# Optimization experiments

Hardware: AMD Instinct MI355X
Metric: run time of the kernel (lower is better)

The kernel has to match this reference:

```python
import jax, jax.numpy as jnp
import numpy as np

HEADS = 16
DIM_HEAD = 64
WINDOW = 128
LOOK_BACKWARD = 1
LOOK_FORWARD = 0
THETA = 10000.0
PAD_VALUE = -1


def look_around(x, backward, forward, pad_value, axis):
    """Gather overlapping windows: concat shifted copies along the intra-window axis."""
    w = x.shape[axis]
    size = backward + forward + 1
    pads = [(0, 0)] * x.ndim
    pads[axis] = (backward, forward)
    p = jnp.pad(x, pads, constant_values=pad_value)
    segs = [jax.lax.slice_in_dim(p, s, s + w, axis=axis) for s in range(size)]
    return jnp.concatenate(segs, axis=axis + 1)


def rotate_half(t):
    t1, t2 = jnp.split(t, 2, axis=-1)
    return jnp.concatenate([-t2, t1], axis=-1)


def setup_inputs() -> dict:
    key = jax.random.key(0)
    k1, k2, k3 = jax.random.split(key, 3)
    dim = 1024
    x = jax.random.normal(k1, (4, 4096, dim), dtype=jnp.float32)
    W_qkv = jax.random.normal(k2, (dim, 3 * HEADS * DIM_HEAD), dtype=jnp.float32) * (dim ** -0.5)
    W_out = jax.random.normal(k3, (HEADS * DIM_HEAD, dim), dtype=jnp.float32) * ((HEADS * DIM_HEAD) ** -0.5)
    return {"x": x, "W_qkv": W_qkv, "W_out": W_out}


def reference(x, W_qkv, W_out):
    b, n, dim = x.shape
    h, dh, ws = HEADS, DIM_HEAD, WINDOW
    w = n // ws
    j = ws * (LOOK_BACKWARD + LOOK_FORWARD + 1)  # 256 keys per query window

    qkv = x @ W_qkv  # (b, n, 3*h*dh)
    q, k, v = jnp.split(qkv, 3, axis=-1)

    def to_bhwnd(t):
        return t.reshape(b, n, h, dh).transpose(0, 2, 1, 3).reshape(b, h, w, ws, dh)

    bq = to_bhwnd(q) * (dh ** -0.5)
    bk = look_around(to_bhwnd(k), LOOK_BACKWARD, LOOK_FORWARD, float(PAD_VALUE), axis=2)
    bv = look_around(to_bhwnd(v), LOOK_BACKWARD, LOOK_FORWARD, float(PAD_VALUE), axis=2)

    # rotary embeddings over the look-around key length; queries use last ws positions
    inv_freq = 1.0 / (THETA ** (jnp.arange(0, dh, 2, dtype=jnp.float32) / dh))
    t_pos = jnp.arange(j, dtype=jnp.float32)
    freqs = t_pos[:, None] * inv_freq[None, :]
    freqs = jnp.concatenate([freqs, freqs], axis=-1)  # (j, dh)
    q_freqs = freqs[-ws:]
    bq = bq * jnp.cos(q_freqs) + rotate_half(bq) * jnp.sin(q_freqs)
    bk = bk * jnp.cos(freqs) + rotate_half(bk) * jnp.sin(freqs)

    sim = jnp.einsum('bhwid,bhwjd->bhwij', bq, bk)  # (b,h,w,ws,j)

    seq = jnp.arange(n).reshape(w, ws)
    bq_t = seq[:, :, None]  # (w, ws, 1)
    bq_k = look_around(seq[None], LOOK_BACKWARD, LOOK_FORWARD, PAD_VALUE, axis=1)[0]  # (w, j)
    bq_k = bq_k[:, None, :]  # (w, 1, j)
    pad_mask = bq_k == PAD_VALUE
    # causal + exact window (look_backward * window_size)
    causal_mask = (bq_t < bq_k) | (bq_t > bq_k + ws * LOOK_BACKWARD)
    mask = causal_mask | pad_mask

    mask_value = -jnp.finfo(sim.dtype).max
    sim = jnp.where(mask, mask_value, sim)
    attn = jax.nn.softmax(sim, axis=-1)

    out = jnp.einsum('bhwij,bhwjd->bhwid', attn, bv)
    out = out.reshape(b, h, n, dh).transpose(0, 2, 1, 3).reshape(b, n, h * dh)
    return out @ W_out
```

## Files before the change

### kernel.cpp

```cpp
#include <hip/hip_runtime.h>
#include <stdint.h>


typedef __attribute__((ext_vector_type(8))) short bfrag;
typedef __attribute__((ext_vector_type(4))) float f4;

#define MFMA_BF16(a, b, c) __builtin_amdgcn_mfma_f32_16x16x32_bf16((a), (b), (c), 0, 0, 0)

static __device__ __forceinline__ short f2bf(float f) {
  unsigned u = __builtin_bit_cast(unsigned, f);
  u = (u + 0x7fffu + ((u >> 16) & 1u)) >> 16;
  return (short)u;
}
static __device__ __forceinline__ float bf2f(short s) {
  unsigned u = ((unsigned)(unsigned short)s) << 16;
  return __builtin_bit_cast(float, u);
}

typedef __attribute__((address_space(3))) unsigned lds_u;
typedef __attribute__((address_space(1))) unsigned gbl_u;

static __device__ __forceinline__ void gl_lds16(const void* g, const void* lds) {
  unsigned loff = (unsigned)__builtin_amdgcn_readfirstlane((int)(uintptr_t)lds);
  __builtin_amdgcn_global_load_lds((gbl_u*)(uintptr_t)g, (lds_u*)(uintptr_t)loff, 16, 0, 0);
}

__global__ __launch_bounds__(256) void convert_x(const float* __restrict__ x,
                                                 short* __restrict__ xb) {
  int idx = blockIdx.x * 256 + threadIdx.x;
  size_t base = (size_t)idx * 8;
  float4 a = *(const float4*)(x + base);
  float4 b = *(const float4*)(x + base + 4);
  bfrag o;
  o[0] = f2bf(a.x); o[1] = f2bf(a.y); o[2] = f2bf(a.z); o[3] = f2bf(a.w);
  o[4] = f2bf(b.x); o[5] = f2bf(b.y); o[6] = f2bf(b.z); o[7] = f2bf(b.w);
  *(bfrag*)(xb + base) = o;
}

__global__ __launch_bounds__(256) void transpose_w(
    const float* __restrict__ wqkv, const float* __restrict__ wout,
    short* __restrict__ wqkvT, short* __restrict__ woutT) {
  __shared__ short t[64][72];
  const int tid = threadIdx.x;
  const int kt = blockIdx.x, yt = blockIdx.y;
  const float* src; short* dst; int N, nt;
  if (yt < 48) { src = wqkv; dst = wqkvT; N = 3072; nt = yt; }
  else         { src = wout; dst = woutT; N = 1024; nt = yt - 48; }
  const int k0 = kt * 64, n0 = nt * 64;
#pragma unroll
  for (int i = 0; i < 4; ++i) {
    int r = i * 16 + (tid >> 4);
    int c = (tid & 15) * 4;
    float4 v = *(const float4*)(src + (size_t)(k0 + r) * N + n0 + c);
    t[c + 0][r] = f2bf(v.x);
    t[c + 1][r] = f2bf(v.y);
    t[c + 2][r] = f2bf(v.z);
    t[c + 3][r] = f2bf(v.w);
  }
  __syncthreads();
#pragma unroll
  for (int i = 0; i < 2; ++i) {
    int c = tid + i * 256;
    int n = c >> 3, k8 = (c & 7) * 8;
    *(bfrag*)(dst + (size_t)(n0 + n) * 1024 + k0 + k8) = *(const bfrag*)&t[n][k8];
  }
}

#define VM4 asm volatile("s_waitcnt vmcnt(4)" ::: "memory")
#define VM0 asm volatile("s_waitcnt vmcnt(0)" ::: "memory")
#define VNOP ((void)0)

#define ST_A(buf, ks, kk)                                                          \
  do {                                                                             \
    gl_lds16(aS0 + (ks) * 32 + (kk), ldsA + (buf) * 32768 + (ks) * 16384 + stA);   \
    gl_lds16(aS1 + (ks) * 32 + (kk),                                               \
             ldsA + (buf) * 32768 + (ks) * 16384 + 8192 + stA);                    \
  } while (0)
#define ST_B(buf, ks, kk)                                                          \
  do {                                                                             \
    gl_lds16(bS0 + (ks) * 32 + (kk), ldsB + (buf) * 32768 + (ks) * 16384 + stA);   \
    gl_lds16(bS1 + (ks) * 32 + (kk),                                               \
             ldsB + (buf) * 32768 + (ks) * 16384 + 8192 + stA);                    \
  } while (0)
#define ST2(buf, ks, kk) do { ST_A(buf, ks, kk); ST_B(buf, ks, kk); } while (0)

#define MM4(mi, a)                                 \
  acc[mi][0] = MFMA_BF16(a, b0, acc[mi][0]);       \
  acc[mi][1] = MFMA_BF16(a, b1, acc[mi][1]);       \
  acc[mi][2] = MFMA_BF16(a, b2, acc[mi][2]);       \
  acc[mi][3] = MFMA_BF16(a, b3, acc[mi][3])

#define PHASE2(buf, ks, STAGE, WAIT)                                               \
  {                                                                                \
    const char* pA_ = ldsA + (buf) * 32768 + (ks) * 16384 + aRd;                   \
    const char* pB_ = ldsB + (buf) * 32768 + (ks) * 16384 + bRd;                   \
    bfrag a0 = *(const bfrag*)(pA_);                                               \
    bfrag a1 = *(const bfrag*)(pA_ + 1024);                                        \
    bfrag a2 = *(const bfrag*)(pA_ + 2048);                                        \
    bfrag a3 = *(const bfrag*)(pA_ + 3072);                                        \
    bfrag a4 = *(const bfrag*)(pA_ + 4096);                                        \
    bfrag a5 = *(const bfrag*)(pA_ + 5120);                                        \
    bfrag a6 = *(const bfrag*)(pA_ + 6144);                                        \
    bfrag a7 = *(const bfrag*)(pA_ + 7168);                                        \
    bfrag b0 = *(const bfrag*)(pB_);                                               \
    bfrag b1 = *(const bfrag*)(pB_ + 1024);                                        \
    bfrag b2 = *(const bfrag*)(pB_ + 2048);                                        \
    bfrag b3 = *(const bfrag*)(pB_ + 3072);                                        \
    STAGE;                                                                         \
    WAIT;                                                                          \
    __builtin_amdgcn_s_barrier();                                                  \
    asm volatile("s_waitcnt lgkmcnt(0)" ::: "memory");                             \
    __builtin_amdgcn_sched_barrier(0);                                             \
    __builtin_amdgcn_s_setprio(1);                                                 \
    MM4(0, a0);                                                                    \
    MM4(1, a1);                                                                    \
    MM4(2, a2);                                                                    \
    MM4(3, a3);                                                                    \
    MM4(4, a4);                                                                    \
    MM4(5, a5);                                                                    \
    MM4(6, a6);                                                                    \
    MM4(7, a7);                                                                    \
    __builtin_amdgcn_s_setprio(0);                                                 \
  }

template <int MODE, int NBX>
__global__ __launch_bounds__(512, 2) void gemm256(
    const short* __restrict__ A, const short* __restrict__ Bt, float* __restrict__ C,
    short* __restrict__ oq, short* __restrict__ ok, short* __restrict__ ov) {
  __shared__ __align__(1024) char lds[131072];
  char* const ldsA = lds;
  char* const ldsB = lds + 65536;

  const int tid = threadIdx.x, lane = tid & 63, wv = tid >> 6;
  const int wr = wv >> 2, wc = wv & 3;
  const int l15 = lane & 15, quad = lane >> 4;

  const int nwg = NBX * 64;
  const int bid = (int)blockIdx.x;
  const int wgid = (bid & 7) * (nwg >> 3) + (bid >> 3);
  const int bx = wgid % NBX, by = wgid / NBX;

  const short* Ab = A + (size_t)by * 256 * 1024;
  const short* Bb = Bt + (size_t)bx * 256 * 1024;

  const int srow = lane & 15, scg = lane >> 4;
  const short* aS0 = Ab + (size_t)(wv * 16 + srow) * 1024 + scg * 8;
  const short* aS1 = Ab + (size_t)((8 + wv) * 16 + srow) * 1024 + scg * 8;
  const short* bS0 = Bb + (size_t)(wv * 16 + srow) * 1024 + scg * 8;
  const short* bS1 = Bb + (size_t)((8 + wv) * 16 + srow) * 1024 + scg * 8;
  const int stA = wv * 1024;

  const int aRd = wr * 8192 + lane * 16;
  const int bRd = wc * 4096 + lane * 16;

  f4 acc[8][4];
#pragma unroll
  for (int i = 0; i < 8; ++i)
#pragma unroll
    for (int j = 0; j < 4; ++j) acc[i][j] = (f4)0.f;

  ST2(0, 0, 0); ST2(0, 1, 0);
  VM4;
  __builtin_amdgcn_s_barrier();

#pragma unroll 1
  for (int t = 0; t < 14; t += 2) {
    const int kn = t * 64 + 64, kn2 = t * 64 + 128;
    PHASE2(0, 0, ST2(1, 0, kn), VM4);
    PHASE2(0, 1, ST2(1, 1, kn), VM4);
    PHASE2(1, 0, ST2(0, 0, kn2), VM4);
    PHASE2(1, 1, ST2(0, 1, kn2), VM4);
  }

  PHASE2(0, 0, ST2(1, 0, 960), VM4);
  PHASE2(0, 1, ST2(1, 1, 960), VM4);
  PHASE2(1, 0, VNOP, VM0);
  PHASE2(1, 1, VNOP, VNOP);

  if constexpr (MODE == 0) {
    const int n64 = bx * 256 + wc * 64;
    const int part = n64 >> 10;
    const int head = (n64 & 1023) >> 6;
    short* o = (part == 0) ? oq : (part == 1) ? ok : ov;
    const int mbase = by * 256 + wr * 128;
    const int bb = mbase >> 12;
    const int p0 = (mbase & 4095) + quad * 4;
    short* const obase = o + (size_t)(bb * 16 + head) * 4096 * 64;
    if (part == 2) {
#pragma unroll
      for (int i = 0; i < 8; ++i)
#pragma unroll
        for (int r = 0; r < 4; ++r) {
          short* row = obase + (size_t)(p0 + i * 16 + r) * 64;
#pragma unroll
          for (int j = 0; j < 4; ++j) row[j * 16 + l15] = f2bf(acc[i][j][r]);
        }
    } else {
      const float qs = (part == 0) ? 0.125f : 1.0f;
      float fr[2], c1[2], s1[2], cD[2], sD[2], cs[2], sn[2];
      fr[0] = exp2f((float)l15 * -0.41524101186f);
      fr[1] = exp2f((float)(16 + l15) * -0.41524101186f);
#pragma unroll
      for (int j = 0; j < 2; ++j) {
        __sincosf(fr[j], &s1[j], &c1[j]);
        __sincosf(13.0f * fr[j], &sD[j], &cD[j]);
        __sincosf((float)p0 * fr[j], &sn[j], &cs[j]);
      }
#pragma unroll
      for (int i = 0; i < 8; ++i) {
#pragma unroll
        for (int r = 0; r < 4; ++r) {
          short* row = obase + (size_t)(p0 + i * 16 + r) * 64;
#pragma unroll
          for (int j = 0; j < 2; ++j) {
            float av = acc[i][j][r], bv2 = acc[i][j + 2][r];
            float ra = (av * cs[j] - bv2 * sn[j]) * qs;
            float rb = (bv2 * cs[j] + av * sn[j]) * qs;
            row[j * 16 + l15] = f2bf(ra);
            row[32 + j * 16 + l15] = f2bf(rb);
          }
          if (r < 3) {
#pragma unroll
            for (int j = 0; j < 2; ++j) {
              float nc = cs[j] * c1[j] - sn[j] * s1[j];
              sn[j] = sn[j] * c1[j] + cs[j] * s1[j];
              cs[j] = nc;
            }
          }
        }
#pragma unroll
        for (int j = 0; j < 2; ++j) {
          float nc = cs[j] * cD[j] - sn[j] * sD[j];
          sn[j] = sn[j] * cD[j] + cs[j] * sD[j];
          cs[j] = nc;
        }
      }
    }
  } else {
#pragma unroll
    for (int i = 0; i < 8; ++i)
#pragma unroll
      for (int j = 0; j < 4; ++j)
#pragma unroll
        for (int r = 0; r < 4; ++r) {
          int m = by * 256 + wr * 128 + i * 16 + quad * 4 + r;
          int n = bx * 256 + wc * 64 + j * 16 + l15;
          C[(size_t)m * 1024 + n] = acc[i][j][r];
        }
  }
}

__global__ __launch_bounds__(256) void attn_kernel(
    const short* __restrict__ qb, const short* __restrict__ kb,
    const short* __restrict__ vb, short* __restrict__ ob) {
  constexpr int KST = 72, VST = 264, PST = 136;
  __shared__ __align__(16) short smem[18432 + 16896];
  short* Ks = smem;
  short* Pl = smem;
  short* Vt = smem + 18432;

  const int bid = blockIdx.x;
  const int w = bid & 31, bh = bid >> 5;
  const int tid = threadIdx.x, lane = tid & 63, wv = tid >> 6;
  const int l15 = lane & 15, quad = lane >> 4;
  const size_t kvbase = (size_t)bh * (4096 * 64);
  const int pk0 = w * 128 - 128;

  const int i0 = wv * 32;
  const short* qbase = qb + kvbase + (size_t)(w * 128) * 64;
  bfrag aq[2][2];
#pragma unroll
  for (int rt = 0; rt < 2; ++rt)
#pragma unroll
    for (int ks = 0; ks < 2; ++ks)
      aq[rt][ks] = *(const bfrag*)(qbase + (size_t)(i0 + rt * 16 + l15) * 64 + ks * 32 + quad * 8);

#pragma unroll
  for (int i = 0; i < 8; ++i) {
    int c = tid + i * 256;
    int row = c >> 3;
    int d0 = (c & 7) * 8;
    int pk = pk0 + row;
    if (pk < 0) pk = 0;
    const size_t src = kvbase + (size_t)pk * 64 + d0;
    bfrag kvv = *(const bfrag*)(kb + src);
    *(bfrag*)&Ks[row * KST + d0] = kvv;
    bfrag vvv = *(const bfrag*)(vb + src);
#pragma unroll
    for (int j = 0; j < 8; ++j) Vt[(d0 + j) * VST + row] = vvv[j];
  }
  __syncthreads();

  f4 sim[2][16];
#pragma unroll
  for (int rt = 0; rt < 2; ++rt)
#pragma unroll
    for (int ct = 0; ct < 16; ++ct) sim[rt][ct] = (f4)0.f;

#pragma unroll
  for (int ct = 0; ct < 16; ++ct) {
    bfrag bk0 = *(const bfrag*)&Ks[(ct * 16 + l15) * KST + quad * 8];
    bfrag bk1 = *(const bfrag*)&Ks[(ct * 16 + l15) * KST + 32 + quad * 8];
#pragma unroll
    for (int rt = 0; rt < 2; ++rt) {
      sim[rt][ct] = MFMA_BF16(aq[rt][0], bk0, sim[rt][ct]);
      sim[rt][ct] = MFMA_BF16(aq[rt][1], bk1, sim[rt][ct]);
    }
  }
  __syncthreads();

  float linv[2][4];
#pragma unroll
  for (int rt = 0; rt < 2; ++rt)
#pragma unroll
    for (int r = 0; r < 4; ++r) {
      const int iloc = i0 + rt * 16 + quad * 4 + r;
      float sum = 0.f;
#pragma unroll
      for (int ct = 0; ct < 16; ++ct) {
        int jj = ct * 16 + l15;
        bool valid = (jj >= iloc) && (jj <= iloc + 128) && ((w > 0) || (jj >= 128));
        float pv = valid ? __expf(sim[rt][ct][r]) : 0.f;
        sim[rt][ct][r] = pv;
        sum += pv;
      }
#pragma unroll
      for (int off = 1; off < 16; off <<= 1) sum += __shfl_xor(sum, off);
      linv[rt][r] = 1.f / sum;
    }

  f4 oacc[2][4];
#pragma unroll
  for (int rt = 0; rt < 2; ++rt)
#pragma unroll
    for (int ctd = 0; ctd < 4; ++ctd) oacc[rt][ctd] = (f4)0.f;

#pragma unroll
  for (int pass = 0; pass < 2; ++pass) {
#pragma unroll
    for (int rt = 0; rt < 2; ++rt)
#pragma unroll
      for (int ct = 0; ct < 8; ++ct) {
        int ctg = pass * 8 + ct;
#pragma unroll
        for (int r = 0; r < 4; ++r)
          Pl[(i0 + rt * 16 + quad * 4 + r) * PST + ct * 16 + l15] = f2bf(sim[rt][ctg][r]);
      }
#pragma unroll
    for (int ks = 0; ks < 4; ++ks) {
      bfrag ap[2];
#pragma unroll
      for (int rt = 0; rt < 2; ++rt)
        ap[rt] = *(const bfrag*)&Pl[(i0 + rt * 16 + l15) * PST + ks * 32 + quad * 8];
#pragma unroll
      for (int ctd = 0; ctd < 4; ++ctd) {
        bfrag bv = *(const bfrag*)&Vt[(ctd * 16 + l15) * VST + pass * 128 + ks * 32 + quad * 8];
#pragma unroll
        for (int rt = 0; rt < 2; ++rt) oacc[rt][ctd] = MFMA_BF16(ap[rt], bv, oacc[rt][ctd]);
      }
    }
  }

  const int b = bh >> 4, h = bh & 15;
  short* obase = ob + ((size_t)b * 4096 + w * 128) * 1024 + h * 64;
#pragma unroll
  for (int rt = 0; rt < 2; ++rt)
#pragma unroll
    for (int ctd = 0; ctd < 4; ++ctd)
#pragma unroll
      for (int r = 0; r < 4; ++r) {
        int i = i0 + rt * 16 + quad * 4 + r;
        int d = ctd * 16 + l15;
        obase[(size_t)i * 1024 + d] = f2bf(oacc[rt][ctd][r] * linv[rt][r]);
      }
}

extern "C" void kernel_launch(void* const* d_in, const int* in_sizes, int n_in,
                              void* d_out, int out_size, void* d_ws, size_t ws_size,
                              hipStream_t stream) {
  const float* x = (const float*)d_in[0];
  const float* wqkv = (const float*)d_in[1];
  const float* wout = (const float*)d_in[2];
  float* out = (float*)d_out;
  char* ws = (char*)d_ws;

  short* qb = (short*)(ws + 0);
  short* kb = (short*)(ws + 33554432);
  short* vb = (short*)(ws + 67108864);
  short* xb = (short*)(ws + 100663296);
  short* ab = xb;
  short* wqkvT = (short*)(ws + 134217728);
  short* woutT = (short*)(ws + 140509184);

  convert_x<<<8192, 256, 0, stream>>>(x, xb);
  transpose_w<<<dim3(16, 64), 256, 0, stream>>>(wqkv, wout, wqkvT, woutT);
  gemm256<0, 12><<<768, 512, 0, stream>>>(xb, wqkvT, nullptr, qb, kb, vb);
  attn_kernel<<<2048, 256, 0, stream>>>(qb, kb, vb, ab);
  gemm256<1, 4><<<256, 512, 0, stream>>>(ab, woutT, out, nullptr, nullptr, nullptr);
}
```

Measured before the change: 356.0 us.

## Software-pipeline LDS fragment loads with MFMA via register double buffering

Restructures the GEMM main loop so the LDS reads for the next k-slice are issued into a second register buffer while MFMAs run on the current one, with sched_group_barriers interleaving them. The global-to-LDS staging is reorganised into a three-stage ring (32-wide k slices prefetched one step further ahead). This is meant to hide LDS read latency behind matrix math and cut the stall after each barrier. In exchange it doubles the fragment registers, which may pressure the 2-waves-per-SIMD occupancy, and the tighter buffer reuse makes correctness depend on careful barrier ordering.

```diff
diff --git a/kernel.cpp b/kernel.cpp
--- a/kernel.cpp
+++ b/kernel.cpp
@@ -72,54 +72,62 @@
 
 #define ST_A(buf, ks, kk)                                                          \
   do {                                                                             \
-    gl_lds16(aS0 + (ks) * 32 + (kk), ldsA + (buf) * 32768 + (ks) * 16384 + stA);   \
-    gl_lds16(aS1 + (ks) * 32 + (kk),                                               \
-             ldsA + (buf) * 32768 + (ks) * 16384 + 8192 + stA);                    \
+    gl_lds16(aS0 + (kk), ldsA + (buf) * 32768 + (ks) * 16384 + stA);               \
+    gl_lds16(aS1 + (kk), ldsA + (buf) * 32768 + (ks) * 16384 + 8192 + stA);        \
   } while (0)
 #define ST_B(buf, ks, kk)                                                          \
   do {                                                                             \
-    gl_lds16(bS0 + (ks) * 32 + (kk), ldsB + (buf) * 32768 + (ks) * 16384 + stA);   \
-    gl_lds16(bS1 + (ks) * 32 + (kk),                                               \
-             ldsB + (buf) * 32768 + (ks) * 16384 + 8192 + stA);                    \
+    gl_lds16(bS0 + (kk), ldsB + (buf) * 32768 + (ks) * 16384 + stA);               \
+    gl_lds16(bS1 + (kk), ldsB + (buf) * 32768 + (ks) * 16384 + 8192 + stA);        \
   } while (0)
 #define ST2(buf, ks, kk) do { ST_A(buf, ks, kk); ST_B(buf, ks, kk); } while (0)
 
-#define MM4(mi, a)                                 \
-  acc[mi][0] = MFMA_BF16(a, b0, acc[mi][0]);       \
-  acc[mi][1] = MFMA_BF16(a, b1, acc[mi][1]);       \
-  acc[mi][2] = MFMA_BF16(a, b2, acc[mi][2]);       \
-  acc[mi][3] = MFMA_BF16(a, b3, acc[mi][3])
-
-#define PHASE2(buf, ks, STAGE, WAIT)                                               \
+#define MM4(R, mi)                                            \
+  acc[mi][0] = MFMA_BF16(fa[R][mi], fb[R][0], acc[mi][0]);    \
+  acc[mi][1] = MFMA_BF16(fa[R][mi], fb[R][1], acc[mi][1]);    \
+  acc[mi][2] = MFMA_BF16(fa[R][mi], fb[R][2], acc[mi][2]);    \
+  acc[mi][3] = MFMA_BF16(fa[R][mi], fb[R][3], acc[mi][3])
+
+#define SGB_MFMA __builtin_amdgcn_sched_group_barrier(0x8, 8, 0)
+#define SGB_DS   __builtin_amdgcn_sched_group_barrier(0x100, 4, 0)
+
+#define PH(R, S, nbuf, nks, STAGE, WAIT)                                           \
   {                                                                                \
-    const char* pA_ = ldsA + (buf) * 32768 + (ks) * 16384 + aRd;                   \
-    const char* pB_ = ldsB + (buf) * 32768 + (ks) * 16384 + bRd;                   \
-    bfrag a0 = *(const bfrag*)(pA_);                                               \
-    bfrag a1 = *(const bfrag*)(pA_ + 1024);                                        \
-    bfrag a2 = *(const bfrag*)(pA_ + 2048);                                        \
-    bfrag a3 = *(const bfrag*)(pA_ + 3072);                                        \
-    bfrag a4 = *(const bfrag*)(pA_ + 4096);                                        \
-    bfrag a5 = *(const bfrag*)(pA_ + 5120);                                        \
-    bfrag a6 = *(const bfrag*)(pA_ + 6144);                                        \
-    bfrag a7 = *(const bfrag*)(pA_ + 7168);                                        \
-    bfrag b0 = *(const bfrag*)(pB_);                                               \
-    bfrag b1 = *(const bfrag*)(pB_ + 1024);                                        \
-    bfrag b2 = *(const bfrag*)(pB_ + 2048);                                        \
-    bfrag b3 = *(const bfrag*)(pB_ + 3072);                                        \
+    const char* nA_ = ldsA + (nbuf) * 32768 + (nks) * 16384 + aRd;                 \
+    const char* nB_ = ldsB + (nbuf) * 32768 + (nks) * 16384 + bRd;                 \
+    asm volatile("s_waitcnt lgkmcnt(0)" ::: "memory");                             \
+    __builtin_amdgcn_sched_barrier(0);                                             \
+    __builtin_amdgcn_s_setprio(1);                                                 \
+    MM4(R, 0); MM4(R, 1);                                                          \
+    fa[S][0] = *(const bfrag*)(nA_);                                               \
+    fa[S][1] = *(const bfrag*)(nA_ + 1024);                                        \
+    fa[S][2] = *(const bfrag*)(nA_ + 2048);                                        \
+    fa[S][3] = *(const bfrag*)(nA_ + 3072);                                        \
+    MM4(R, 2); MM4(R, 3);                                                          \
+    fa[S][4] = *(const bfrag*)(nA_ + 4096);                                        \
+    fa[S][5] = *(const bfrag*)(nA_ + 5120);                                        \
+    fa[S][6] = *(const bfrag*)(nA_ + 6144);                                        \
+    fa[S][7] = *(const bfrag*)(nA_ + 7168);                                        \
+    MM4(R, 4); MM4(R, 5);                                                          \
+    fb[S][0] = *(const bfrag*)(nB_);                                               \
+    fb[S][1] = *(const bfrag*)(nB_ + 1024);                                        \
+    fb[S][2] = *(const bfrag*)(nB_ + 2048);                                        \
+    fb[S][3] = *(const bfrag*)(nB_ + 3072);                                        \
+    MM4(R, 6); MM4(R, 7);                                                          \
+    SGB_MFMA; SGB_DS; SGB_MFMA; SGB_DS; SGB_MFMA; SGB_DS; SGB_MFMA;                \
+    __builtin_amdgcn_s_setprio(0);                                                 \
     STAGE;                                                                         \
     WAIT;                                                                          \
     __builtin_amdgcn_s_barrier();                                                  \
+  }
+
+#define PH_LAST(R)                                                                 \
+  {                                                                                \
     asm volatile("s_waitcnt lgkmcnt(0)" ::: "memory");                             \
     __builtin_amdgcn_sched_barrier(0);                                             \
     __builtin_amdgcn_s_setprio(1);                                                 \
-    MM4(0, a0);                                                                    \
-    MM4(1, a1);                                                                    \
-    MM4(2, a2);                                                                    \
-    MM4(3, a3);                                                                    \
-    MM4(4, a4);                                                                    \
-    MM4(5, a5);                                                                    \
-    MM4(6, a6);                                                                    \
-    MM4(7, a7);                                                                    \
+    MM4(R, 0); MM4(R, 1); MM4(R, 2); MM4(R, 3);                                    \
+    MM4(R, 4); MM4(R, 5); MM4(R, 6); MM4(R, 7);                                    \
     __builtin_amdgcn_s_setprio(0);                                                 \
   }
 
@@ -159,23 +167,43 @@
 #pragma unroll
     for (int j = 0; j < 4; ++j) acc[i][j] = (f4)0.f;
 
-  ST2(0, 0, 0); ST2(0, 1, 0);
+  bfrag fa[2][8];
+  bfrag fb[2][4];
+
+  ST2(0, 0, 0); ST2(0, 1, 32); ST2(1, 0, 64);
   VM4;
   __builtin_amdgcn_s_barrier();
+  {
+    const char* pA0 = ldsA + aRd;
+    const char* pB0 = ldsB + bRd;
+    fa[0][0] = *(const bfrag*)(pA0);
+    fa[0][1] = *(const bfrag*)(pA0 + 1024);
+    fa[0][2] = *(const bfrag*)(pA0 + 2048);
+    fa[0][3] = *(const bfrag*)(pA0 + 3072);
+    fa[0][4] = *(const bfrag*)(pA0 + 4096);
+    fa[0][5] = *(const bfrag*)(pA0 + 5120);
+    fa[0][6] = *(const bfrag*)(pA0 + 6144);
+    fa[0][7] = *(const bfrag*)(pA0 + 7168);
+    fb[0][0] = *(const bfrag*)(pB0);
+    fb[0][1] = *(const bfrag*)(pB0 + 1024);
+    fb[0][2] = *(const bfrag*)(pB0 + 2048);
+    fb[0][3] = *(const bfrag*)(pB0 + 3072);
+  }
 
 #pragma unroll 1
-  for (int t = 0; t < 14; t += 2) {
-    const int kn = t * 64 + 64, kn2 = t * 64 + 128;
-    PHASE2(0, 0, ST2(1, 0, kn), VM4);
-    PHASE2(0, 1, ST2(1, 1, kn), VM4);
-    PHASE2(1, 0, ST2(0, 0, kn2), VM4);
-    PHASE2(1, 1, ST2(0, 1, kn2), VM4);
-  }
-
-  PHASE2(0, 0, ST2(1, 0, 960), VM4);
-  PHASE2(0, 1, ST2(1, 1, 960), VM4);
-  PHASE2(1, 0, VNOP, VM0);
-  PHASE2(1, 1, VNOP, VNOP);
+  for (int i = 0; i < 7; ++i) {
+    const int k3 = i * 128 + 96, k4 = i * 128 + 128;
+    const int k5 = i * 128 + 160, k6 = i * 128 + 192;
+    PH(0, 1, 0, 1, ST2(1, 1, k3), VM4);
+    PH(1, 0, 1, 0, ST2(0, 0, k4), VM4);
+    PH(0, 1, 1, 1, ST2(0, 1, k5), VM4);
+    PH(1, 0, 0, 0, ST2(1, 0, k6), VM4);
+  }
+
+  PH(0, 1, 0, 1, ST2(1, 1, 992), VM4);
+  PH(1, 0, 1, 0, VNOP, VM0);
+  PH(0, 1, 1, 1, VNOP, VNOP);
+  PH_LAST(1);
 
   if constexpr (MODE == 0) {
     const int n64 = bx * 256 + wc * 64;
```

Result: slower. 494.2 us (+38.8%).
